# Kernel tuning notes

Hardware: AMD Instinct MI355X
Metric: run time of the kernel (lower is better)

The kernel has to match this reference:

```python
import jax, jax.numpy as jnp
import numpy as np

N = 25000
E = 400000
H = 4        # heads
C = 256      # per-head channels
D_IN = 1024
NEG_SLOPE = 0.2


def setup_inputs() -> dict:
    key = jax.random.key(0)
    k1, k2, k3, k4, k5, k6 = jax.random.split(key, 6)
    x = jax.random.normal(k1, (N, D_IN), dtype=jnp.float32)
    edge_index = jax.random.randint(k2, (2, E), 0, N, dtype=jnp.int64)
    # GATConv parameters
    scale = 1.0 / np.sqrt(D_IN)
    W = jax.random.normal(k3, (D_IN, H * C), dtype=jnp.float32) * scale
    att_src = jax.random.normal(k4, (H, C), dtype=jnp.float32) * 0.1
    att_dst = jax.random.normal(k5, (H, C), dtype=jnp.float32) * 0.1
    bias = jax.random.normal(k6, (H * C,), dtype=jnp.float32) * 0.01
    return {"x": x, "edge_index": edge_index, "W": W,
            "att_src": att_src, "att_dst": att_dst, "bias": bias}


def reference(x, edge_index, W, att_src, att_dst, bias):
    # Dense projection: [N, D_IN] @ [D_IN, H*C] -> [N, H, C]
    xp = (x @ W).reshape(N, H, C)

    # Per-node attention logits [N, H]
    a_src = jnp.einsum('nhc,hc->nh', xp, att_src)
    a_dst = jnp.einsum('nhc,hc->nh', xp, att_dst)

    # PyG default add_self_loops=True
    loops = jnp.arange(N, dtype=edge_index.dtype)
    src = jnp.concatenate([edge_index[0], loops])  # [E+N]
    dst = jnp.concatenate([edge_index[1], loops])  # [E+N]

    # Edge attention logits + LeakyReLU
    e = jax.nn.leaky_relu(a_src[src] + a_dst[dst], NEG_SLOPE)  # [E+N, H]

    # Segment softmax over destination nodes (every node has a self loop)
    m = jax.ops.segment_max(e, dst, num_segments=N)            # [N, H]
    ee = jnp.exp(e - m[dst])
    z = jax.ops.segment_sum(ee, dst, num_segments=N)           # [N, H]
    alpha = ee / z[dst]                                        # [E+N, H]

    # Scatter-weighted aggregation: out[i] = sum_j alpha_ij * xp[j]
    msgs = xp[src] * alpha[:, :, None]                         # [E+N, H, C]
    out = jax.ops.segment_sum(msgs, dst, num_segments=N)       # [N, H, C]

    out = out.reshape(N, H * C) + bias
    # dropout(0.5) is identity in eval mode; act = ReLU
    return jax.nn.relu(out)
```

## Files before the change

kernel.cpp:

```cpp
#include <hip/hip_runtime.h>
#include <hip/hip_bf16.h>
#include <stdint.h>

#define N_NODES 25000
#define M_PAD   25088
#define E_EDGES 400000
#define NE      (E_EDGES + N_NODES)
#define HEADS   4
#define D_DIM   1024
#define NEG_SLOPE 0.2f
#define NBLK_SCAN ((N_NODES + 255) / 256)

using bf16x8  = __attribute__((ext_vector_type(8))) short;
using floatx4 = __attribute__((ext_vector_type(4))) float;

__device__ __forceinline__ unsigned short f2bf(float f) {
    union { float f; unsigned u; } v{f};
    unsigned r = v.u + 0x7fffu + ((v.u >> 16) & 1u);
    return (unsigned short)(r >> 16);
}
__device__ __forceinline__ float bf2f(unsigned short s) {
    union { unsigned u; float f; } v{(unsigned)s << 16};
    return v.f;
}

__global__ __launch_bounds__(256) void k_convert_x(
        const float* __restrict__ x, unsigned short* __restrict__ xb) {
    int i = blockIdx.x * 256 + threadIdx.x;
    int row = i >> 8;
    if (row >= M_PAD) return;
    ushort4 o;
    if (row < N_NODES) {
        float4 v = ((const float4*)x)[i];
        o = make_ushort4(f2bf(v.x), f2bf(v.y), f2bf(v.z), f2bf(v.w));
    } else {
        o = make_ushort4(0, 0, 0, 0);
    }
    ((ushort4*)xb)[i] = o;
}

__global__ void k_convert_wt(const float* __restrict__ W,
                             unsigned short* __restrict__ Wt) {
    __shared__ float tile[32][33];
    int bx = blockIdx.x, by = blockIdx.y;
    int tx = threadIdx.x, ty = threadIdx.y;
    #pragma unroll
    for (int i = 0; i < 32; i += 8) {
        int k = by * 32 + ty + i;
        int n = bx * 32 + tx;
        tile[ty + i][tx] = W[(size_t)k * D_DIM + n];
    }
    __syncthreads();
    #pragma unroll
    for (int i = 0; i < 32; i += 8) {
        int n = bx * 32 + ty + i;
        int k = by * 32 + tx;
        Wt[(size_t)n * D_DIM + k] = f2bf(tile[tx][ty + i]);
    }
}

__global__ __launch_bounds__(256) void k_gemm(
        const unsigned short* __restrict__ A,
        const unsigned short* __restrict__ Bt,
        unsigned short* __restrict__ C) {
    __shared__ __align__(16) unsigned short As[128 * 32];
    __shared__ __align__(16) unsigned short Bs[128 * 32];

    const int tid  = threadIdx.x;
    const int m0   = blockIdx.x * 128;
    const int n0   = blockIdx.y * 128;
    const int wave = tid >> 6, lane = tid & 63;
    const int wm   = (wave & 1) * 64, wn = (wave >> 1) * 64;
    const int lrow = lane & 15;
    const int quad = lane >> 4;

    floatx4 acc[4][4] = {};

    for (int k0 = 0; k0 < D_DIM; k0 += 32) {
        #pragma unroll
        for (int s = 0; s < 2; ++s) {
            int q  = tid + s * 256;
            int r  = q >> 2;
            int c8 = (q & 3) * 8;
            *(int4*)(&As[r * 32 + c8]) =
                *(const int4*)(&A[(size_t)(m0 + r) * D_DIM + k0 + c8]);
            *(int4*)(&Bs[r * 32 + c8]) =
                *(const int4*)(&Bt[(size_t)(n0 + r) * D_DIM + k0 + c8]);
        }
        __syncthreads();

        bf16x8 af[4], bfr[4];
        #pragma unroll
        for (int mi = 0; mi < 4; ++mi)
            af[mi] = *(const bf16x8*)(&As[(wm + mi * 16 + lrow) * 32 + quad * 8]);
        #pragma unroll
        for (int ni = 0; ni < 4; ++ni)
            bfr[ni] = *(const bf16x8*)(&Bs[(wn + ni * 16 + lrow) * 32 + quad * 8]);

        #pragma unroll
        for (int mi = 0; mi < 4; ++mi)
            #pragma unroll
            for (int ni = 0; ni < 4; ++ni)
                acc[mi][ni] = __builtin_amdgcn_mfma_f32_16x16x32_bf16(
                    af[mi], bfr[ni], acc[mi][ni], 0, 0, 0);
        __syncthreads();
    }

    #pragma unroll
    for (int mi = 0; mi < 4; ++mi) {
        #pragma unroll
        for (int ni = 0; ni < 4; ++ni) {
            #pragma unroll
            for (int r = 0; r < 4; ++r) {
                int gm = m0 + wm + mi * 16 + quad * 4 + r;
                int gn = n0 + wn + ni * 16 + lrow;
                C[(size_t)gm * D_DIM + gn] = f2bf(acc[mi][ni][r]);
            }
        }
    }
}

__global__ __launch_bounds__(256) void k_node_logits(
        const unsigned short* __restrict__ xp,
        const float* __restrict__ att_src, const float* __restrict__ att_dst,
        float* __restrict__ a_src, float* __restrict__ a_dst) {
    int n = blockIdx.x;
    int tid = threadIdx.x;
    int h = tid >> 6, lane = tid & 63;
    int c = h * 256 + lane * 4;
    ushort4 v  = *(const ushort4*)(&xp[(size_t)n * D_DIM + c]);
    float4 as  = *(const float4*)(&att_src[c]);
    float4 ad  = *(const float4*)(&att_dst[c]);
    float x0 = bf2f(v.x), x1 = bf2f(v.y), x2 = bf2f(v.z), x3 = bf2f(v.w);
    float s = x0 * as.x + x1 * as.y + x2 * as.z + x3 * as.w;
    float d = x0 * ad.x + x1 * ad.y + x2 * ad.z + x3 * ad.w;
    #pragma unroll
    for (int off = 32; off > 0; off >>= 1) {
        s += __shfl_down(s, off);
        d += __shfl_down(d, off);
    }
    if (lane == 0) { a_src[n * 4 + h] = s; a_dst[n * 4 + h] = d; }
}

__global__ __launch_bounds__(256) void k_deg(
        const int* __restrict__ ei, int* __restrict__ deg) {
    int e = blockIdx.x * 256 + threadIdx.x;
    if (e >= NE) return;
    int d = (e < E_EDGES) ? ei[E_EDGES + e] : (e - E_EDGES);
    atomicAdd(&deg[d], 1);
}

__global__ __launch_bounds__(256) void k_scan1(
        const int* __restrict__ deg, int* __restrict__ rowstart,
        int* __restrict__ blocksum) {
    __shared__ int smem[256];
    int i = blockIdx.x * 256 + threadIdx.x;
    int v = (i < N_NODES) ? deg[i] : 0;
    smem[threadIdx.x] = v;
    __syncthreads();
    #pragma unroll
    for (int off = 1; off < 256; off <<= 1) {
        int t = (threadIdx.x >= off) ? smem[threadIdx.x - off] : 0;
        __syncthreads();
        smem[threadIdx.x] += t;
        __syncthreads();
    }
    if (i < N_NODES) rowstart[i] = smem[threadIdx.x] - v;
    if (threadIdx.x == 255) blocksum[blockIdx.x] = smem[255];
}

__global__ __launch_bounds__(128) void k_scan2(
        const int* __restrict__ blocksum, int* __restrict__ blockoff) {
    __shared__ int smem[128];
    int v = (threadIdx.x < NBLK_SCAN) ? blocksum[threadIdx.x] : 0;
    smem[threadIdx.x] = v;
    __syncthreads();
    #pragma unroll
    for (int off = 1; off < 128; off <<= 1) {
        int t = (threadIdx.x >= off) ? smem[threadIdx.x - off] : 0;
        __syncthreads();
        smem[threadIdx.x] += t;
        __syncthreads();
    }
    blockoff[threadIdx.x] = smem[threadIdx.x] - v;
}

__global__ __launch_bounds__(256) void k_scan3(
        int* __restrict__ rowstart, const int* __restrict__ blockoff) {
    int i = blockIdx.x * 256 + threadIdx.x;
    if (i < N_NODES) rowstart[i] += blockoff[blockIdx.x];
    if (i == 0) rowstart[N_NODES] = NE;
}

__global__ __launch_bounds__(256) void k_edge_exp_scatter(
        const int* __restrict__ ei,
        const float* __restrict__ a_src, const float* __restrict__ a_dst,
        const int* __restrict__ rowstart, int* __restrict__ cursor,
        int* __restrict__ csr_src, float* __restrict__ csr_ee) {
    int e = blockIdx.x * 256 + threadIdx.x;
    if (e >= NE) return;
    int s, d;
    if (e < E_EDGES) { s = ei[e]; d = ei[E_EDGES + e]; }
    else             { s = d = e - E_EDGES; }
    float4 as = *(const float4*)(&a_src[s * 4]);
    float4 ad = *(const float4*)(&a_dst[d * 4]);
    float l0 = as.x + ad.x, l1 = as.y + ad.y, l2 = as.z + ad.z, l3 = as.w + ad.w;
    l0 = l0 > 0.f ? l0 : NEG_SLOPE * l0;
    l1 = l1 > 0.f ? l1 : NEG_SLOPE * l1;
    l2 = l2 > 0.f ? l2 : NEG_SLOPE * l2;
    l3 = l3 > 0.f ? l3 : NEG_SLOPE * l3;
    int pos  = atomicAdd(&cursor[d], 1);
    int slot = rowstart[d] + pos;
    csr_src[slot] = s;
    *(float4*)(&csr_ee[(size_t)slot * 4]) =
        make_float4(__expf(l0), __expf(l1), __expf(l2), __expf(l3));
}

__global__ __launch_bounds__(256) void k_node_aggregate(
        const int* __restrict__ csr_src, const float* __restrict__ csr_ee,
        const int* __restrict__ rowstart,
        const unsigned short* __restrict__ xp,
        const float* __restrict__ bias, float* __restrict__ out) {
    int n   = blockIdx.x;
    int tid = threadIdx.x;
    int row = rowstart[n];
    int deg = rowstart[n + 1] - row;

    __shared__ float zsh[4];
    if (tid < 64) {
        float z0 = 0.f, z1 = 0.f, z2 = 0.f, z3 = 0.f;
        for (int i = tid; i < deg; i += 64) {
            float4 v = *(const float4*)(&csr_ee[(size_t)(row + i) * 4]);
            z0 += v.x; z1 += v.y; z2 += v.z; z3 += v.w;
        }
        #pragma unroll
        for (int off = 32; off > 0; off >>= 1) {
            z0 += __shfl_down(z0, off);
            z1 += __shfl_down(z1, off);
            z2 += __shfl_down(z2, off);
            z3 += __shfl_down(z3, off);
        }
        if (tid == 0) { zsh[0] = z0; zsh[1] = z1; zsh[2] = z2; zsh[3] = z3; }
    }
    __syncthreads();

    int h = tid >> 6;
    int c = tid * 4;
    float rz = 1.0f / zsh[h];
    float a0 = 0.f, a1 = 0.f, a2 = 0.f, a3 = 0.f;
    for (int i = 0; i < deg; ++i) {
        int s   = csr_src[row + i];
        float a = csr_ee[(size_t)(row + i) * 4 + h] * rz;
        ushort4 v = *(const ushort4*)(&xp[(size_t)s * D_DIM + c]);
        a0 += a * bf2f(v.x);
        a1 += a * bf2f(v.y);
        a2 += a * bf2f(v.z);
        a3 += a * bf2f(v.w);
    }
    float4 b = *(const float4*)(&bias[c]);
    float4 o;
    o.x = fmaxf(a0 + b.x, 0.f);
    o.y = fmaxf(a1 + b.y, 0.f);
    o.z = fmaxf(a2 + b.z, 0.f);
    o.w = fmaxf(a3 + b.w, 0.f);
    *(float4*)(&out[(size_t)n * D_DIM + c]) = o;
}

extern "C" void kernel_launch(void* const* d_in, const int* in_sizes, int n_in,
                              void* d_out, int out_size, void* d_ws, size_t ws_size,
                              hipStream_t stream) {
    const float* x       = (const float*)d_in[0];
    const int*   ei      = (const int*)d_in[1];
    const float* W       = (const float*)d_in[2];
    const float* att_src = (const float*)d_in[3];
    const float* att_dst = (const float*)d_in[4];
    const float* bias    = (const float*)d_in[5];
    float* out = (float*)d_out;

    char* ws = (char*)d_ws;
    size_t off = 0;
    auto alloc = [&](size_t bytes) -> void* {
        void* p = ws + off;
        off = (off + bytes + 255) & ~(size_t)255;
        return p;
    };
    unsigned short* xb   = (unsigned short*)alloc((size_t)M_PAD * D_DIM * 2);
    unsigned short* Wt   = (unsigned short*)alloc((size_t)D_DIM * D_DIM * 2);
    unsigned short* xpb  = (unsigned short*)alloc((size_t)M_PAD * D_DIM * 2);
    float* a_src    = (float*)alloc((size_t)N_NODES * 4 * 4);
    float* a_dst    = (float*)alloc((size_t)N_NODES * 4 * 4);
    int*   deg      = (int*)alloc((size_t)N_NODES * 4);
    int*   rowstart = (int*)alloc((size_t)(N_NODES + 1) * 4);
    int*   cursor   = (int*)alloc((size_t)N_NODES * 4);
    int*   blocksum = (int*)alloc((size_t)NBLK_SCAN * 4);
    int*   blockoff = (int*)alloc((size_t)128 * 4);
    int*   csr_src  = (int*)alloc((size_t)NE * 4);
    float* csr_ee   = (float*)alloc((size_t)NE * 4 * 4);

    hipMemsetAsync(deg, 0, (size_t)N_NODES * 4, stream);
    hipMemsetAsync(cursor, 0, (size_t)N_NODES * 4, stream);

    k_convert_x<<<M_PAD, 256, 0, stream>>>(x, xb);
    k_convert_wt<<<dim3(32, 32), dim3(32, 8), 0, stream>>>(W, Wt);
    k_gemm<<<dim3(M_PAD / 128, D_DIM / 128), 256, 0, stream>>>(xb, Wt, xpb);
    k_node_logits<<<N_NODES, 256, 0, stream>>>(xpb, att_src, att_dst, a_src, a_dst);
    k_deg<<<(NE + 255) / 256, 256, 0, stream>>>(ei, deg);
    k_scan1<<<NBLK_SCAN, 256, 0, stream>>>(deg, rowstart, blocksum);
    k_scan2<<<1, 128, 0, stream>>>(blocksum, blockoff);
    k_scan3<<<NBLK_SCAN, 256, 0, stream>>>(rowstart, blockoff);
    k_edge_exp_scatter<<<(NE + 255) / 256, 256, 0, stream>>>(
        ei, a_src, a_dst, rowstart, cursor, csr_src, csr_ee);
    k_node_aggregate<<<N_NODES, 256, 0, stream>>>(
        csr_src, csr_ee, rowstart, xpb, bias, out);
}
```

Before: 467.9 us.

## Use direct global-to-LDS loads in GEMM and widen aggregation to two nodes per block

The GEMM tile staging now uses the global_load_lds builtin, which writes global data straight into shared memory instead of going through registers. The aggregation kernel now handles two nodes per 256-thread block, with 128 threads per node. Each thread reads 8 bf16 channels per gather, and the edge loop is unrolled by 4 so several gathers are in flight at once. The aim is to cut register staging in the GEMM and to raise memory-level parallelism in the gather-bound aggregation, at the cost of more registers per thread and a block that now depends on two nodes' degrees.

Measured after the change: 465.0 us. No clear change (-0.6%).

```diff
diff --git a/kernel.cpp b/kernel.cpp
--- a/kernel.cpp
+++ b/kernel.cpp
@@ -13,6 +13,7 @@
 
 using bf16x8  = __attribute__((ext_vector_type(8))) short;
 using floatx4 = __attribute__((ext_vector_type(4))) float;
+using ushort8 = __attribute__((ext_vector_type(8))) unsigned short;
 
 __device__ __forceinline__ unsigned short f2bf(float f) {
     union { float f; unsigned u; } v{f};
@@ -74,18 +75,27 @@
     const int lrow = lane & 15;
     const int quad = lane >> 4;
 
+    const int srow = (lane >> 2);
+    const int scol = (lane & 3) * 8;
+
     floatx4 acc[4][4] = {};
 
     for (int k0 = 0; k0 < D_DIM; k0 += 32) {
         #pragma unroll
-        for (int s = 0; s < 2; ++s) {
-            int q  = tid + s * 256;
-            int r  = q >> 2;
-            int c8 = (q & 3) * 8;
-            *(int4*)(&As[r * 32 + c8]) =
-                *(const int4*)(&A[(size_t)(m0 + r) * D_DIM + k0 + c8]);
-            *(int4*)(&Bs[r * 32 + c8]) =
-                *(const int4*)(&Bt[(size_t)(n0 + r) * D_DIM + k0 + c8]);
+        for (int j = 0; j < 2; ++j) {
+            int rbase = wave * 32 + j * 16;
+            const unsigned short* ga =
+                &A[(size_t)(m0 + rbase + srow) * D_DIM + k0 + scol];
+            const unsigned short* gb =
+                &Bt[(size_t)(n0 + rbase + srow) * D_DIM + k0 + scol];
+            __builtin_amdgcn_global_load_lds(
+                (const __attribute__((address_space(1))) void*)ga,
+                (__attribute__((address_space(3))) void*)&As[rbase * 32],
+                16, 0, 0);
+            __builtin_amdgcn_global_load_lds(
+                (const __attribute__((address_space(1))) void*)gb,
+                (__attribute__((address_space(3))) void*)&Bs[rbase * 32],
+                16, 0, 0);
         }
         __syncthreads();
 
@@ -216,20 +226,28 @@
         make_float4(__expf(l0), __expf(l1), __expf(l2), __expf(l3));
 }
 
+__device__ __forceinline__ void acc8(float* acc, float a, ushort8 v) {
+    #pragma unroll
+    for (int j = 0; j < 8; ++j) acc[j] += a * bf2f((unsigned short)v[j]);
+}
+
 __global__ __launch_bounds__(256) void k_node_aggregate(
         const int* __restrict__ csr_src, const float* __restrict__ csr_ee,
         const int* __restrict__ rowstart,
         const unsigned short* __restrict__ xp,
         const float* __restrict__ bias, float* __restrict__ out) {
-    int n   = blockIdx.x;
-    int tid = threadIdx.x;
-    int row = rowstart[n];
-    int deg = rowstart[n + 1] - row;
-
-    __shared__ float zsh[4];
-    if (tid < 64) {
+    const int tid  = threadIdx.x;
+    const int half = tid >> 7;
+    const int n    = blockIdx.x * 2 + half;
+    const int t    = tid & 127;
+    const int row  = rowstart[n];
+    const int deg  = rowstart[n + 1] - row;
+
+    __shared__ float zsh[2][4];
+    if ((tid & 64) == 0) {
+        int lane = tid & 63;
         float z0 = 0.f, z1 = 0.f, z2 = 0.f, z3 = 0.f;
-        for (int i = tid; i < deg; i += 64) {
+        for (int i = lane; i < deg; i += 64) {
             float4 v = *(const float4*)(&csr_ee[(size_t)(row + i) * 4]);
             z0 += v.x; z1 += v.y; z2 += v.z; z3 += v.w;
         }
@@ -240,30 +258,57 @@
             z2 += __shfl_down(z2, off);
             z3 += __shfl_down(z3, off);
         }
-        if (tid == 0) { zsh[0] = z0; zsh[1] = z1; zsh[2] = z2; zsh[3] = z3; }
+        if (lane == 0) {
+            zsh[half][0] = z0; zsh[half][1] = z1;
+            zsh[half][2] = z2; zsh[half][3] = z3;
+        }
     }
     __syncthreads();
 
-    int h = tid >> 6;
-    int c = tid * 4;
-    float rz = 1.0f / zsh[h];
-    float a0 = 0.f, a1 = 0.f, a2 = 0.f, a3 = 0.f;
-    for (int i = 0; i < deg; ++i) {
+    const int h = t >> 5;
+    const int c = t * 8;
+    const float rz = 1.0f / zsh[half][h];
+
+    float acc[8] = {};
+    int i = 0;
+    for (; i + 4 <= deg; i += 4) {
+        int s0 = csr_src[row + i + 0];
+        int s1 = csr_src[row + i + 1];
+        int s2 = csr_src[row + i + 2];
+        int s3 = csr_src[row + i + 3];
+        float a0 = csr_ee[(size_t)(row + i + 0) * 4 + h] * rz;
+        float a1 = csr_ee[(size_t)(row + i + 1) * 4 + h] * rz;
+        float a2 = csr_ee[(size_t)(row + i + 2) * 4 + h] * rz;
+        float a3 = csr_ee[(size_t)(row + i + 3) * 4 + h] * rz;
+        ushort8 v0 = *(const ushort8*)(&xp[(size_t)s0 * D_DIM + c]);
+        ushort8 v1 = *(const ushort8*)(&xp[(size_t)s1 * D_DIM + c]);
+        ushort8 v2 = *(const ushort8*)(&xp[(size_t)s2 * D_DIM + c]);
+        ushort8 v3 = *(const ushort8*)(&xp[(size_t)s3 * D_DIM + c]);
+        acc8(acc, a0, v0);
+        acc8(acc, a1, v1);
+        acc8(acc, a2, v2);
+        acc8(acc, a3, v3);
+    }
+    for (; i < deg; ++i) {
         int s   = csr_src[row + i];
         float a = csr_ee[(size_t)(row + i) * 4 + h] * rz;
-        ushort4 v = *(const ushort4*)(&xp[(size_t)s * D_DIM + c]);
-        a0 += a * bf2f(v.x);
-        a1 += a * bf2f(v.y);
-        a2 += a * bf2f(v.z);
-        a3 += a * bf2f(v.w);
-    }
-    float4 b = *(const float4*)(&bias[c]);
-    float4 o;
-    o.x = fmaxf(a0 + b.x, 0.f);
-    o.y = fmaxf(a1 + b.y, 0.f);
-    o.z = fmaxf(a2 + b.z, 0.f);
-    o.w = fmaxf(a3 + b.w, 0.f);
-    *(float4*)(&out[(size_t)n * D_DIM + c]) = o;
+        ushort8 v = *(const ushort8*)(&xp[(size_t)s * D_DIM + c]);
+        acc8(acc, a, v);
+    }
+
+    float4 b0 = *(const float4*)(&bias[c]);
+    float4 b1 = *(const float4*)(&bias[c + 4]);
+    float4 o0, o1;
+    o0.x = fmaxf(acc[0] + b0.x, 0.f);
+    o0.y = fmaxf(acc[1] + b0.y, 0.f);
+    o0.z = fmaxf(acc[2] + b0.z, 0.f);
+    o0.w = fmaxf(acc[3] + b0.w, 0.f);
+    o1.x = fmaxf(acc[4] + b1.x, 0.f);
+    o1.y = fmaxf(acc[5] + b1.y, 0.f);
+    o1.z = fmaxf(acc[6] + b1.z, 0.f);
+    o1.w = fmaxf(acc[7] + b1.w, 0.f);
+    *(float4*)(&out[(size_t)n * D_DIM + c])     = o0;
+    *(float4*)(&out[(size_t)n * D_DIM + c + 4]) = o1;
 }
 
 extern "C" void kernel_launch(void* const* d_in, const int* in_sizes, int n_in,
@@ -310,6 +355,6 @@
     k_scan3<<<NBLK_SCAN, 256, 0, stream>>>(rowstart, blockoff);
     k_edge_exp_scatter<<<(NE + 255) / 256, 256, 0, stream>>>(
         ei, a_src, a_dst, rowstart, cursor, csr_src, csr_ee);
-    k_node_aggregate<<<N_NODES, 256, 0, stream>>>(
+    k_node_aggregate<<<12500, 256, 0, stream>>>(
         csr_src, csr_ee, rowstart, xpb, bias, out);
 }
```

## Chunk projected features by channel and schedule aggregation per XCD for L2 reuse

Applied to the files above, without the earlier changes.

The GEMM now writes its output in a channel-chunked layout (16 chunks of 64 columns), and the aggregation kernel is remapped so that each XCD works on two fixed chunks across groups of 16 nodes. The intent is to keep each chunk's gather working set within one XCD's L2 instead of gathering full 2 KB rows. Softmax normalisation moves into a separate k_alpha kernel that writes head-major alpha. The GEMM staging switches to direct global-to-LDS loads, the aggregation loop is unrolled by two, and the two memsets are merged into one. In exchange there is an extra kernel pass and alpha buffer, and the block-to-XCD mapping assumes round-robin dispatch across 8 XCDs.

Result: slower. 481.2 us (+2.8%).

```diff
diff --git a/kernel.cpp b/kernel.cpp
--- a/kernel.cpp
+++ b/kernel.cpp
@@ -10,9 +10,12 @@
 #define D_DIM   1024
 #define NEG_SLOPE 0.2f
 #define NBLK_SCAN ((N_NODES + 255) / 256)
+#define CHUNKS  16
+#define GRP     1563
 
 using bf16x8  = __attribute__((ext_vector_type(8))) short;
 using floatx4 = __attribute__((ext_vector_type(4))) float;
+using ushort8 = __attribute__((ext_vector_type(8))) unsigned short;
 
 __device__ __forceinline__ unsigned short f2bf(float f) {
     union { float f; unsigned u; } v{f};
@@ -74,18 +77,27 @@
     const int lrow = lane & 15;
     const int quad = lane >> 4;
 
+    const int srow = (lane >> 2);
+    const int scol = (lane & 3) * 8;
+
     floatx4 acc[4][4] = {};
 
     for (int k0 = 0; k0 < D_DIM; k0 += 32) {
         #pragma unroll
-        for (int s = 0; s < 2; ++s) {
-            int q  = tid + s * 256;
-            int r  = q >> 2;
-            int c8 = (q & 3) * 8;
-            *(int4*)(&As[r * 32 + c8]) =
-                *(const int4*)(&A[(size_t)(m0 + r) * D_DIM + k0 + c8]);
-            *(int4*)(&Bs[r * 32 + c8]) =
-                *(const int4*)(&Bt[(size_t)(n0 + r) * D_DIM + k0 + c8]);
+        for (int j = 0; j < 2; ++j) {
+            int rbase = wave * 32 + j * 16;
+            const unsigned short* ga =
+                &A[(size_t)(m0 + rbase + srow) * D_DIM + k0 + scol];
+            const unsigned short* gb =
+                &Bt[(size_t)(n0 + rbase + srow) * D_DIM + k0 + scol];
+            __builtin_amdgcn_global_load_lds(
+                (const __attribute__((address_space(1))) void*)ga,
+                (__attribute__((address_space(3))) void*)&As[rbase * 32],
+                16, 0, 0);
+            __builtin_amdgcn_global_load_lds(
+                (const __attribute__((address_space(1))) void*)gb,
+                (__attribute__((address_space(3))) void*)&Bs[rbase * 32],
+                16, 0, 0);
         }
         __syncthreads();
 
@@ -114,21 +126,23 @@
             for (int r = 0; r < 4; ++r) {
                 int gm = m0 + wm + mi * 16 + quad * 4 + r;
                 int gn = n0 + wn + ni * 16 + lrow;
-                C[(size_t)gm * D_DIM + gn] = f2bf(acc[mi][ni][r]);
+                int ch = gn >> 6, sub = gn & 63;
+                C[((size_t)ch * M_PAD + gm) * 64 + sub] = f2bf(acc[mi][ni][r]);
             }
         }
     }
 }
 
 __global__ __launch_bounds__(256) void k_node_logits(
-        const unsigned short* __restrict__ xp,
+        const unsigned short* __restrict__ xp_t,
         const float* __restrict__ att_src, const float* __restrict__ att_dst,
         float* __restrict__ a_src, float* __restrict__ a_dst) {
     int n = blockIdx.x;
     int tid = threadIdx.x;
     int h = tid >> 6, lane = tid & 63;
     int c = h * 256 + lane * 4;
-    ushort4 v  = *(const ushort4*)(&xp[(size_t)n * D_DIM + c]);
+    int ch = c >> 6, sub = c & 63;
+    ushort4 v  = *(const ushort4*)(&xp_t[((size_t)ch * M_PAD + n) * 64 + sub]);
     float4 as  = *(const float4*)(&att_src[c]);
     float4 ad  = *(const float4*)(&att_dst[c]);
     float x0 = bf2f(v.x), x1 = bf2f(v.y), x2 = bf2f(v.z), x3 = bf2f(v.w);
@@ -216,53 +230,93 @@
         make_float4(__expf(l0), __expf(l1), __expf(l2), __expf(l3));
 }
 
+__global__ __launch_bounds__(256) void k_alpha(
+        const float* __restrict__ csr_ee, const int* __restrict__ rowstart,
+        float* __restrict__ alpha) {
+    const int lane = threadIdx.x & 63;
+    const int n    = blockIdx.x * 4 + (threadIdx.x >> 6);
+    const int row  = rowstart[n];
+    const int deg  = rowstart[n + 1] - row;
+
+    float z0 = 0.f, z1 = 0.f, z2 = 0.f, z3 = 0.f;
+    for (int i = lane; i < deg; i += 64) {
+        float4 v = *(const float4*)(&csr_ee[(size_t)(row + i) * 4]);
+        z0 += v.x; z1 += v.y; z2 += v.z; z3 += v.w;
+    }
+    #pragma unroll
+    for (int off = 32; off > 0; off >>= 1) {
+        z0 += __shfl_xor(z0, off);
+        z1 += __shfl_xor(z1, off);
+        z2 += __shfl_xor(z2, off);
+        z3 += __shfl_xor(z3, off);
+    }
+    float r0 = 1.f / z0, r1 = 1.f / z1, r2 = 1.f / z2, r3 = 1.f / z3;
+    for (int i = lane; i < deg; i += 64) {
+        float4 v = *(const float4*)(&csr_ee[(size_t)(row + i) * 4]);
+        alpha[0 * (size_t)NE + row + i] = v.x * r0;
+        alpha[1 * (size_t)NE + row + i] = v.y * r1;
+        alpha[2 * (size_t)NE + row + i] = v.z * r2;
+        alpha[3 * (size_t)NE + row + i] = v.w * r3;
+    }
+}
+
 __global__ __launch_bounds__(256) void k_node_aggregate(
-        const int* __restrict__ csr_src, const float* __restrict__ csr_ee,
+        const int* __restrict__ csr_src, const float* __restrict__ alpha,
         const int* __restrict__ rowstart,
-        const unsigned short* __restrict__ xp,
+        const unsigned short* __restrict__ xp_t,
         const float* __restrict__ bias, float* __restrict__ out) {
-    int n   = blockIdx.x;
-    int tid = threadIdx.x;
-    int row = rowstart[n];
-    int deg = rowstart[n + 1] - row;
-
-    __shared__ float zsh[4];
-    if (tid < 64) {
-        float z0 = 0.f, z1 = 0.f, z2 = 0.f, z3 = 0.f;
-        for (int i = tid; i < deg; i += 64) {
-            float4 v = *(const float4*)(&csr_ee[(size_t)(row + i) * 4]);
-            z0 += v.x; z1 += v.y; z2 += v.z; z3 += v.w;
-        }
-        #pragma unroll
-        for (int off = 32; off > 0; off >>= 1) {
-            z0 += __shfl_down(z0, off);
-            z1 += __shfl_down(z1, off);
-            z2 += __shfl_down(z2, off);
-            z3 += __shfl_down(z3, off);
-        }
-        if (tid == 0) { zsh[0] = z0; zsh[1] = z1; zsh[2] = z2; zsh[3] = z3; }
-    }
-    __syncthreads();
-
-    int h = tid >> 6;
-    int c = tid * 4;
-    float rz = 1.0f / zsh[h];
+    const int b    = blockIdx.x;
+    const int xcd  = b & 7;
+    const int seq  = b >> 3;
+    const int hi   = (seq >= GRP) ? 1 : 0;
+    const int ch   = xcd * 2 + hi;
+    const int grp  = seq - hi * GRP;
+
+    const int t    = threadIdx.x;
+    const int slot = t >> 4;
+    const int sub4 = (t & 15) * 4;
+    const int n    = grp * 16 + slot;
+    if (n >= N_NODES) return;
+
+    const int h   = ch >> 2;
+    const int row = rowstart[n];
+    const int deg = rowstart[n + 1] - row;
+
+    const float* __restrict__ alpha_h = alpha + (size_t)h * NE;
+    const unsigned short* __restrict__ base =
+        xp_t + (size_t)ch * M_PAD * 64 + sub4;
+
     float a0 = 0.f, a1 = 0.f, a2 = 0.f, a3 = 0.f;
-    for (int i = 0; i < deg; ++i) {
-        int s   = csr_src[row + i];
-        float a = csr_ee[(size_t)(row + i) * 4 + h] * rz;
-        ushort4 v = *(const ushort4*)(&xp[(size_t)s * D_DIM + c]);
-        a0 += a * bf2f(v.x);
-        a1 += a * bf2f(v.y);
-        a2 += a * bf2f(v.z);
-        a3 += a * bf2f(v.w);
-    }
-    float4 b = *(const float4*)(&bias[c]);
+    int i = 0;
+    for (; i + 2 <= deg; i += 2) {
+        int   s0 = csr_src[row + i];
+        int   s1 = csr_src[row + i + 1];
+        float w0 = alpha_h[row + i];
+        float w1 = alpha_h[row + i + 1];
+        ushort4 v0 = *(const ushort4*)(base + (size_t)s0 * 64);
+        ushort4 v1 = *(const ushort4*)(base + (size_t)s1 * 64);
+        a0 += w0 * bf2f(v0.x) + w1 * bf2f(v1.x);
+        a1 += w0 * bf2f(v0.y) + w1 * bf2f(v1.y);
+        a2 += w0 * bf2f(v0.z) + w1 * bf2f(v1.z);
+        a3 += w0 * bf2f(v0.w) + w1 * bf2f(v1.w);
+    }
+    if (i < deg) {
+        int   s0 = csr_src[row + i];
+        float w0 = alpha_h[row + i];
+        ushort4 v0 = *(const ushort4*)(base + (size_t)s0 * 64);
+        a0 += w0 * bf2f(v0.x);
+        a1 += w0 * bf2f(v0.y);
+        a2 += w0 * bf2f(v0.z);
+        a3 += w0 * bf2f(v0.w);
+    }
+
+    const int c = ch * 64 + sub4;
+    float4 bv = *(const float4*)(&bias[c]);
     float4 o;
-    o.x = fmaxf(a0 + b.x, 0.f);
-    o.y = fmaxf(a1 + b.y, 0.f);
-    o.z = fmaxf(a2 + b.z, 0.f);
-    o.w = fmaxf(a3 + b.w, 0.f);
+    o.x = fmaxf(a0 + bv.x, 0.f);
+    o.y = fmaxf(a1 + bv.y, 0.f);
+    o.z = fmaxf(a2 + bv.z, 0.f);
+    o.w = fmaxf(a3 + bv.w, 0.f);
     *(float4*)(&out[(size_t)n * D_DIM + c]) = o;
 }
 
@@ -286,30 +340,32 @@
     };
     unsigned short* xb   = (unsigned short*)alloc((size_t)M_PAD * D_DIM * 2);
     unsigned short* Wt   = (unsigned short*)alloc((size_t)D_DIM * D_DIM * 2);
-    unsigned short* xpb  = (unsigned short*)alloc((size_t)M_PAD * D_DIM * 2);
+    unsigned short* xpt  = (unsigned short*)alloc((size_t)M_PAD * D_DIM * 2);
     float* a_src    = (float*)alloc((size_t)N_NODES * 4 * 4);
     float* a_dst    = (float*)alloc((size_t)N_NODES * 4 * 4);
     int*   deg      = (int*)alloc((size_t)N_NODES * 4);
+    int*   cursor   = (int*)alloc((size_t)N_NODES * 4);
     int*   rowstart = (int*)alloc((size_t)(N_NODES + 1) * 4);
-    int*   cursor   = (int*)alloc((size_t)N_NODES * 4);
     int*   blocksum = (int*)alloc((size_t)NBLK_SCAN * 4);
     int*   blockoff = (int*)alloc((size_t)128 * 4);
     int*   csr_src  = (int*)alloc((size_t)NE * 4);
     float* csr_ee   = (float*)alloc((size_t)NE * 4 * 4);
-
-    hipMemsetAsync(deg, 0, (size_t)N_NODES * 4, stream);
-    hipMemsetAsync(cursor, 0, (size_t)N_NODES * 4, stream);
+    float* alpha    = (float*)alloc((size_t)NE * 4 * 4);
+
+    size_t degspan = (size_t)((char*)cursor - (char*)deg) + (size_t)N_NODES * 4;
+    hipMemsetAsync(deg, 0, degspan, stream);
 
     k_convert_x<<<M_PAD, 256, 0, stream>>>(x, xb);
     k_convert_wt<<<dim3(32, 32), dim3(32, 8), 0, stream>>>(W, Wt);
-    k_gemm<<<dim3(M_PAD / 128, D_DIM / 128), 256, 0, stream>>>(xb, Wt, xpb);
-    k_node_logits<<<N_NODES, 256, 0, stream>>>(xpb, att_src, att_dst, a_src, a_dst);
+    k_gemm<<<dim3(M_PAD / 128, D_DIM / 128), 256, 0, stream>>>(xb, Wt, xpt);
+    k_node_logits<<<N_NODES, 256, 0, stream>>>(xpt, att_src, att_dst, a_src, a_dst);
     k_deg<<<(NE + 255) / 256, 256, 0, stream>>>(ei, deg);
     k_scan1<<<NBLK_SCAN, 256, 0, stream>>>(deg, rowstart, blocksum);
     k_scan2<<<1, 128, 0, stream>>>(blocksum, blockoff);
     k_scan3<<<NBLK_SCAN, 256, 0, stream>>>(rowstart, blockoff);
     k_edge_exp_scatter<<<(NE + 255) / 256, 256, 0, stream>>>(
         ei, a_src, a_dst, rowstart, cursor, csr_src, csr_ee);
-    k_node_aggregate<<<N_NODES, 256, 0, stream>>>(
-        csr_src, csr_ee, rowstart, xpb, bias, out);
-}
+    k_alpha<<<6250, 256, 0, stream>>>(csr_ee, rowstart, alpha);
+    k_node_aggregate<<<CHUNKS * GRP, 256, 0, stream>>>(
+        csr_src, alpha, rowstart, xpt, bias, out);
+}
```
